# Performance work log

Hardware: AMD Instinct MI355X
Metric: run time of the kernel (lower is better)

## Reference

```python
import jax, jax.numpy as jnp
import numpy as np

N_NODES = 100000
N_EDGES = 1600000
D = 128
N_CLASS = 10
N_LAYERS = 3
BN_EPS = 1e-5


def setup_inputs() -> dict:
    key = jax.random.key(0)
    ks = jax.random.split(key, 12)
    s = 1.0 / np.sqrt(D)
    x = jax.random.normal(ks[0], (N_NODES, D), dtype=jnp.float32)
    edge_index = jax.random.randint(ks[1], (2, N_EDGES), 0, N_NODES, dtype=jnp.int64)
    return {
        "x": x,
        "edge_index": edge_index,
        "W1": jax.random.normal(ks[2], (N_LAYERS, D, D), dtype=jnp.float32) * s,
        "b1": jnp.zeros((N_LAYERS, D), dtype=jnp.float32),
        "gamma": jnp.ones((N_LAYERS, D), dtype=jnp.float32),
        "beta": jnp.zeros((N_LAYERS, D), dtype=jnp.float32),
        "W2": jax.random.normal(ks[3], (N_LAYERS, D, D), dtype=jnp.float32) * s,
        "b2": jnp.zeros((N_LAYERS, D), dtype=jnp.float32),
        "lin1_W": jax.random.normal(ks[4], (D, D), dtype=jnp.float32) * s,
        "lin1_b": jnp.zeros((D,), dtype=jnp.float32),
        "lin2_W": jax.random.normal(ks[5], (N_CLASS, D), dtype=jnp.float32) * s,
        "lin2_b": jnp.zeros((N_CLASS,), dtype=jnp.float32),
    }


def _gin_layer(h, src, dst, W1, b1, g, bt, W2, b2):
    # GINConv with eps=0: mlp((1+eps)*x + sum_{j->i} x_j)
    agg = jax.ops.segment_sum(h[src], dst, num_segments=N_NODES)  # [N, D]
    z = (h + agg) @ W1.T + b1
    # BatchNorm1d (training-mode batch statistics, biased variance)
    mu = jnp.mean(z, axis=0)
    var = jnp.var(z, axis=0)
    z = (z - mu) * jax.lax.rsqrt(var + BN_EPS) * g + bt
    z = jax.nn.relu(z)
    z = jax.nn.relu(z @ W2.T + b2)
    return z


def reference(x, edge_index, W1, b1, gamma, beta, W2, b2, lin1_W, lin1_b, lin2_W, lin2_b):
    src, dst = edge_index[0], edge_index[1]
    h = x.astype(jnp.float32)
    for i in range(N_LAYERS):
        h = _gin_layer(h, src, dst, W1[i], b1[i], gamma[i], beta[i], W2[i], b2[i])
    h = jax.nn.relu(h @ lin1_W.T + lin1_b)
    h = h @ lin2_W.T + lin2_b
    return jax.nn.sigmoid(h)
```

## Files before the change

kernel.cpp:

```cpp
#include <hip/hip_runtime.h>
#include <math.h>

#define N_NODES 100000
#define N_EDGES 1600000
#define D 128
#define NCLASS 10
#define NLAYERS 3
#define BN_EPS 1e-5f

#define LDA 136
#define BUCKET_SH 7
#define NBUK 782
#define NBLK 256
#define CHUNK 6250
#define SCAN_BLKS NBUK

typedef __attribute__((ext_vector_type(8))) short bf16x8;
typedef __attribute__((ext_vector_type(4))) float f32x4;
typedef __attribute__((ext_vector_type(4))) uint u32x4;

__device__ __forceinline__ ushort f2b(float x) {
    uint u = __float_as_uint(x);
    return (ushort)((u + 0x7fffu + ((u >> 16) & 1u)) >> 16);
}
__device__ __forceinline__ float b2f(uint u) {
    return __uint_as_float(u << 16);
}
__device__ __forceinline__ uint pack2(float a, float b) {
    return (uint)f2b(a) | ((uint)f2b(b) << 16);
}

__global__ __launch_bounds__(256) void k_hist(const int* __restrict__ dst,
                                              int* __restrict__ hist) {
    __shared__ int lh[NBUK];
    int t = threadIdx.x, b = blockIdx.x;
    for (int i = t; i < NBUK; i += 256) lh[i] = 0;
    __syncthreads();
    int e0 = b * CHUNK;
    for (int e = e0 + t; e < e0 + CHUNK; e += 256)
        atomicAdd(&lh[dst[e] >> BUCKET_SH], 1);
    __syncthreads();
    for (int i = t; i < NBUK; i += 256) hist[i * NBLK + b] = lh[i];
}

__global__ __launch_bounds__(256) void k_scan1(int* __restrict__ hist, int* __restrict__ psums) {
    __shared__ int sh[256];
    int t = threadIdx.x;
    int i = blockIdx.x * 256 + t;
    int v = hist[i];
    sh[t] = v; __syncthreads();
    for (int off = 1; off < 256; off <<= 1) {
        int a = (t >= off) ? sh[t - off] : 0;
        __syncthreads();
        sh[t] += a;
        __syncthreads();
    }
    hist[i] = sh[t] - v;
    if (t == 255) psums[blockIdx.x] = sh[255];
}

__global__ __launch_bounds__(1024) void k_scan2(int* __restrict__ psums) {
    __shared__ int sh[1024];
    int t = threadIdx.x;
    int v = (t < SCAN_BLKS) ? psums[t] : 0;
    sh[t] = v; __syncthreads();
    for (int off = 1; off < 1024; off <<= 1) {
        int a = (t >= off) ? sh[t - off] : 0;
        __syncthreads();
        sh[t] += a;
        __syncthreads();
    }
    if (t < SCAN_BLKS) psums[t] = sh[t] - v;
}

__global__ __launch_bounds__(256) void k_partition(const int* __restrict__ src,
                                                   const int* __restrict__ dst,
                                                   const int* __restrict__ hist,
                                                   const int* __restrict__ psums,
                                                   uint* __restrict__ tmp) {
    __shared__ int lcur[NBUK];
    int t = threadIdx.x, b = blockIdx.x;
    for (int i = t; i < NBUK; i += 256) lcur[i] = hist[i * NBLK + b] + psums[i];
    __syncthreads();
    int e0 = b * CHUNK;
    for (int e = e0 + t; e < e0 + CHUNK; e += 256) {
        int d = dst[e];
        int bk = d >> BUCKET_SH;
        int pos = atomicAdd(&lcur[bk], 1);
        tmp[pos] = (uint)src[e] | ((uint)(d & ((1 << BUCKET_SH) - 1)) << 17);
    }
}

__global__ __launch_bounds__(256) void k_bucket_fill(const uint* __restrict__ tmp,
                                                     const int* __restrict__ psums,
                                                     int* __restrict__ row_ptr,
                                                     int* __restrict__ csr) {
    __shared__ int hist[128], inc[128], cur[128];
    int b = blockIdx.x, t = threadIdx.x;
    int base = psums[b];
    int end  = (b + 1 < NBUK) ? psums[b + 1] : N_EDGES;
    int nb = end - base;
    int lo = b << BUCKET_SH;
    const uint* bt = tmp + base;

    if (t < 128) hist[t] = 0;
    __syncthreads();
    for (int i = t; i < nb; i += 256)
        atomicAdd(&hist[bt[i] >> 17], 1);
    __syncthreads();
    if (t < 128) inc[t] = hist[t];
    __syncthreads();
    for (int offs = 1; offs < 128; offs <<= 1) {
        int a = (t < 128 && t >= offs) ? inc[t - offs] : 0;
        __syncthreads();
        if (t < 128) inc[t] += a;
        __syncthreads();
    }
    if (t < 128) {
        int node = lo + t;
        if (node < N_NODES) row_ptr[node] = base + inc[t] - hist[t];
        cur[t] = 0;
    }
    if (b == NBUK - 1 && t == 0) row_ptr[N_NODES] = base + nb;
    __syncthreads();
    for (int i = t; i < nb; i += 256) {
        uint u = bt[i];
        int dl = u >> 17;
        int s = (int)(u & 0x1ffffu);
        int p = atomicAdd(&cur[dl], 1);
        csr[base + (inc[dl] - hist[dl]) + p] = s;
    }
}

__global__ void k_conv(const float* __restrict__ x, const float* __restrict__ W1,
                       const float* __restrict__ W2, const float* __restrict__ l1W,
                       ushort* __restrict__ hbf, ushort* __restrict__ wbf) {
    int i = blockIdx.x * 256 + threadIdx.x;
    const int n4x = N_NODES * D / 4;
    if (i < n4x) {
        float4 v = ((const float4*)x)[i];
        uint2 u;
        u.x = pack2(v.x, v.y);
        u.y = pack2(v.z, v.w);
        ((uint2*)hbf)[i] = u;
    } else {
        int k = i - n4x;
        const float* srcp;
        ushort* dstp;
        if (k < 12288)      { srcp = W1 + k * 4;            dstp = wbf + k * 4; }
        else if (k < 24576) { srcp = W2 + (k - 12288) * 4;  dstp = wbf + 49152 + (k - 12288) * 4; }
        else if (k < 28672) { srcp = l1W + (k - 24576) * 4; dstp = wbf + 98304 + (k - 24576) * 4; }
        else return;
        float4 v = *(const float4*)srcp;
        ushort4 u;
        u.x = f2b(v.x); u.y = f2b(v.y); u.z = f2b(v.z); u.w = f2b(v.w);
        *(ushort4*)dstp = u;
    }
}

__global__ __launch_bounds__(256) void k_aggregate(const ushort* __restrict__ hbf,
                                                   const int* __restrict__ row_ptr,
                                                   const int* __restrict__ csr,
                                                   ushort* __restrict__ outbf) {
    int node = blockIdx.x * 4 + (threadIdx.x >> 6);
    int lane = threadIdx.x & 63;
    const uint* hp = (const uint*)hbf;
    uint self = hp[(size_t)node * 64 + lane];
    float ax = b2f(self & 0xffffu), ay = b2f(self >> 16);
    int e0 = row_ptr[node], e1 = row_ptr[node + 1];
    int e = e0;
    for (; e + 7 < e1; e += 8) {
        uint v0 = hp[(size_t)csr[e]     * 64 + lane];
        uint v1 = hp[(size_t)csr[e + 1] * 64 + lane];
        uint v2 = hp[(size_t)csr[e + 2] * 64 + lane];
        uint v3 = hp[(size_t)csr[e + 3] * 64 + lane];
        uint v4 = hp[(size_t)csr[e + 4] * 64 + lane];
        uint v5 = hp[(size_t)csr[e + 5] * 64 + lane];
        uint v6 = hp[(size_t)csr[e + 6] * 64 + lane];
        uint v7 = hp[(size_t)csr[e + 7] * 64 + lane];
        ax += b2f(v0 & 0xffffu); ay += b2f(v0 >> 16);
        ax += b2f(v1 & 0xffffu); ay += b2f(v1 >> 16);
        ax += b2f(v2 & 0xffffu); ay += b2f(v2 >> 16);
        ax += b2f(v3 & 0xffffu); ay += b2f(v3 >> 16);
        ax += b2f(v4 & 0xffffu); ay += b2f(v4 >> 16);
        ax += b2f(v5 & 0xffffu); ay += b2f(v5 >> 16);
        ax += b2f(v6 & 0xffffu); ay += b2f(v6 >> 16);
        ax += b2f(v7 & 0xffffu); ay += b2f(v7 >> 16);
    }
    for (; e < e1; ++e) {
        uint v = hp[(size_t)csr[e] * 64 + lane];
        ax += b2f(v & 0xffffu); ay += b2f(v >> 16);
    }
    __builtin_nontemporal_store(pack2(ax, ay), (uint*)outbf + (size_t)node * 64 + lane);
}

template <int PRE, int POST, int STATS>
__global__ __launch_bounds__(256, 4) void k_gemm(const ushort* __restrict__ inA,
                                                 const ushort* __restrict__ Wbf,
                                                 const float* __restrict__ bias,
                                                 const float* __restrict__ scale,
                                                 const float* __restrict__ shift,
                                                 ushort* __restrict__ outp,
                                                 float* __restrict__ gsum,
                                                 float* __restrict__ gsq,
                                                 int nrows) {
    __shared__ ushort sA[128 * LDA];
    __shared__ float sbias[128];
    __shared__ float lsum[128], lsq[128];

    int t = threadIdx.x;
    int r0 = blockIdx.x * 128;

    if (t < 128) {
        sbias[t] = bias[t];
        lsum[t] = 0.f; lsq[t] = 0.f;
    }

    for (int idx = t; idx < 128 * 16; idx += 256) {
        int r = idx >> 4, c8 = (idx & 15) << 3;
        int rr = r0 + r;
        u32x4 v = (u32x4){0u, 0u, 0u, 0u};
        if (rr < nrows) v = __builtin_nontemporal_load((const u32x4*)(inA + (size_t)rr * 128 + c8));
        if (PRE == 2) {
            float f0 = b2f(v.x & 0xffffu), f1 = b2f(v.x >> 16);
            float f2 = b2f(v.y & 0xffffu), f3 = b2f(v.y >> 16);
            float f4 = b2f(v.z & 0xffffu), f5 = b2f(v.z >> 16);
            float f6 = b2f(v.w & 0xffffu), f7 = b2f(v.w >> 16);
            float4 sc0 = *(const float4*)(scale + c8);
            float4 sc1 = *(const float4*)(scale + c8 + 4);
            float4 sf0 = *(const float4*)(shift + c8);
            float4 sf1 = *(const float4*)(shift + c8 + 4);
            f0 = fmaxf(fmaf(f0, sc0.x, sf0.x), 0.f);
            f1 = fmaxf(fmaf(f1, sc0.y, sf0.y), 0.f);
            f2 = fmaxf(fmaf(f2, sc0.z, sf0.z), 0.f);
            f3 = fmaxf(fmaf(f3, sc0.w, sf0.w), 0.f);
            f4 = fmaxf(fmaf(f4, sc1.x, sf1.x), 0.f);
            f5 = fmaxf(fmaf(f5, sc1.y, sf1.y), 0.f);
            f6 = fmaxf(fmaf(f6, sc1.z, sf1.z), 0.f);
            f7 = fmaxf(fmaf(f7, sc1.w, sf1.w), 0.f);
            v.x = pack2(f0, f1); v.y = pack2(f2, f3);
            v.z = pack2(f4, f5); v.w = pack2(f6, f7);
        }
        *(u32x4*)&sA[r * LDA + c8] = v;
    }
    __syncthreads();

    int lane = t & 63, wid = t >> 6;
    int rl = lane & 15, g = lane >> 4;
    int wr = wid >> 1, wc = wid & 1;

    f32x4 acc[4][4];
#pragma unroll
    for (int i = 0; i < 4; ++i)
#pragma unroll
        for (int j = 0; j < 4; ++j) acc[i][j] = (f32x4){0.f, 0.f, 0.f, 0.f};

#pragma unroll
    for (int ks = 0; ks < 4; ++ks) {
        int koff = ks * 32 + g * 8;
        bf16x8 a[4], b[4];
#pragma unroll
        for (int ni = 0; ni < 4; ++ni)
            b[ni] = *(const bf16x8*)&Wbf[(size_t)(wc * 64 + ni * 16 + rl) * 128 + koff];
#pragma unroll
        for (int mi = 0; mi < 4; ++mi)
            a[mi] = *(const bf16x8*)&sA[(wr * 64 + mi * 16 + rl) * LDA + koff];
#pragma unroll
        for (int mi = 0; mi < 4; ++mi)
#pragma unroll
            for (int ni = 0; ni < 4; ++ni)
                acc[mi][ni] = __builtin_amdgcn_mfma_f32_16x16x32_bf16(a[mi], b[ni], acc[mi][ni], 0, 0, 0);
    }

    float bn[4], ssum[4], ssq[4];
#pragma unroll
    for (int ni = 0; ni < 4; ++ni) {
        bn[ni] = sbias[wc * 64 + ni * 16 + rl];
        ssum[ni] = 0.f; ssq[ni] = 0.f;
    }

#pragma unroll
    for (int mi = 0; mi < 4; ++mi) {
        int orow = r0 + wr * 64 + mi * 16 + g * 4;
#pragma unroll
        for (int j = 0; j < 4; ++j) {
            int row = orow + j;
            if (row < nrows) {
#pragma unroll
                for (int ni = 0; ni < 4; ++ni) {
                    int ocol = wc * 64 + ni * 16 + rl;
                    float o = acc[mi][ni][j] + bn[ni];
                    if (STATS) { ssum[ni] += o; ssq[ni] += o * o; }
                    if (POST) o = fmaxf(o, 0.f);
                    outp[(size_t)row * 128 + ocol] = f2b(o);
                }
            }
        }
    }

    if (STATS) {
#pragma unroll
        for (int ni = 0; ni < 4; ++ni) {
            float s = ssum[ni], q = ssq[ni];
            s += __shfl_xor(s, 16, 64); q += __shfl_xor(q, 16, 64);
            s += __shfl_xor(s, 32, 64); q += __shfl_xor(q, 32, 64);
            if (g == 0) {
                int col = wc * 64 + ni * 16 + rl;
                atomicAdd(&lsum[col], s);
                atomicAdd(&lsq[col], q);
            }
        }
        __syncthreads();
        if (t < 128) {
            atomicAdd(&gsum[t], lsum[t]);
            atomicAdd(&gsq[t], lsq[t]);
        }
    }
}

__global__ void k_bnfin(float* __restrict__ gsum, float* __restrict__ gsq,
                        const float* __restrict__ gamma, const float* __restrict__ beta,
                        float* __restrict__ scale, float* __restrict__ shift) {
    int d = threadIdx.x;
    float s = gsum[d], q = gsq[d];
    float mu = s * (1.f / N_NODES);
    float var = q * (1.f / N_NODES) - mu * mu;
    float rstd = rsqrtf(var + BN_EPS);
    float sc = rstd * gamma[d];
    scale[d] = sc;
    shift[d] = beta[d] - mu * sc;
    gsum[d] = 0.f;
    gsq[d] = 0.f;
}

__global__ __launch_bounds__(256, 3) void k_head(const ushort* __restrict__ hbf,
                                                 const ushort* __restrict__ l1bf,
                                                 const float* __restrict__ b1f,
                                                 const float* __restrict__ W2,
                                                 const float* __restrict__ b2f_,
                                                 float* __restrict__ out) {
    __shared__ ushort sA[128 * LDA];
    __shared__ float sbias[128];
    __shared__ float w2s[NCLASS * 128];
    __shared__ float b2s[NCLASS];

    int t = threadIdx.x;
    int r0 = blockIdx.x * 128;

    if (t < 128) sbias[t] = b1f[t];
    for (int idx = t; idx < (NCLASS * 128) / 4; idx += 256)
        *(float4*)&w2s[idx * 4] = *(const float4*)(W2 + idx * 4);
    if (t < NCLASS) b2s[t] = b2f_[t];

    for (int idx = t; idx < 128 * 16; idx += 256) {
        int r = idx >> 4, c8 = (idx & 15) << 3;
        int rr = r0 + r;
        u32x4 v = (u32x4){0u, 0u, 0u, 0u};
        if (rr < N_NODES) v = __builtin_nontemporal_load((const u32x4*)(hbf + (size_t)rr * 128 + c8));
        *(u32x4*)&sA[r * LDA + c8] = v;
    }
    __syncthreads();

    int lane = t & 63, wid = t >> 6;
    int rl = lane & 15, g = lane >> 4;
    int wr = wid >> 1, wc = wid & 1;

    f32x4 acc[4][4];
#pragma unroll
    for (int i = 0; i < 4; ++i)
#pragma unroll
        for (int j = 0; j < 4; ++j) acc[i][j] = (f32x4){0.f, 0.f, 0.f, 0.f};

#pragma unroll
    for (int ks = 0; ks < 4; ++ks) {
        int koff = ks * 32 + g * 8;
        bf16x8 a[4], b[4];
#pragma unroll
        for (int ni = 0; ni < 4; ++ni)
            b[ni] = *(const bf16x8*)&l1bf[(size_t)(wc * 64 + ni * 16 + rl) * 128 + koff];
#pragma unroll
        for (int mi = 0; mi < 4; ++mi)
            a[mi] = *(const bf16x8*)&sA[(wr * 64 + mi * 16 + rl) * LDA + koff];
#pragma unroll
        for (int mi = 0; mi < 4; ++mi)
#pragma unroll
            for (int ni = 0; ni < 4; ++ni)
                acc[mi][ni] = __builtin_amdgcn_mfma_f32_16x16x32_bf16(a[mi], b[ni], acc[mi][ni], 0, 0, 0);
    }

    __syncthreads();

    float bn[4];
#pragma unroll
    for (int ni = 0; ni < 4; ++ni) bn[ni] = sbias[wc * 64 + ni * 16 + rl];
#pragma unroll
    for (int mi = 0; mi < 4; ++mi) {
        int rowl = wr * 64 + mi * 16 + g * 4;
#pragma unroll
        for (int j = 0; j < 4; ++j) {
#pragma unroll
            for (int ni = 0; ni < 4; ++ni) {
                int ocol = wc * 64 + ni * 16 + rl;
                float o = fmaxf(acc[mi][ni][j] + bn[ni], 0.f);
                sA[ocol * LDA + rowl + j] = f2b(o);
            }
        }
    }
    __syncthreads();

    int row = t & 127, ch = t >> 7;
    float acc2[5] = {0.f, 0.f, 0.f, 0.f, 0.f};
    const float* w2p = &w2s[ch * 5 * 128];
#pragma unroll 4
    for (int k = 0; k < 128; ++k) {
        float v = b2f(sA[k * LDA + row]);
#pragma unroll
        for (int c = 0; c < 5; ++c)
            acc2[c] = fmaf(v, w2p[c * 128 + k], acc2[c]);
    }
    int rr = r0 + row;
    if (rr < N_NODES) {
#pragma unroll
        for (int c = 0; c < 5; ++c) {
            float z = acc2[c] + b2s[ch * 5 + c];
            out[(size_t)rr * NCLASS + ch * 5 + c] = 1.f / (1.f + expf(-z));
        }
    }
}

extern "C" void kernel_launch(void* const* d_in, const int* in_sizes, int n_in,
                              void* d_out, int out_size, void* d_ws, size_t ws_size,
                              hipStream_t stream) {
    const float* x     = (const float*)d_in[0];
    const int*   ei    = (const int*)d_in[1];
    const float* W1    = (const float*)d_in[2];
    const float* b1    = (const float*)d_in[3];
    const float* gamma = (const float*)d_in[4];
    const float* beta  = (const float*)d_in[5];
    const float* W2    = (const float*)d_in[6];
    const float* b2    = (const float*)d_in[7];
    const float* l1W   = (const float*)d_in[8];
    const float* l1b   = (const float*)d_in[9];
    const float* l2W   = (const float*)d_in[10];
    const float* l2b   = (const float*)d_in[11];
    float* out = (float*)d_out;

    char* w = (char*)d_ws;
    ushort* hbf    = (ushort*)(w);
    ushort* zbf    = (ushort*)(w + 25600000);
    ushort* aggout = (ushort*)(w + 51200000);
    int*   row_ptr = (int*)   (w + 76800000);
    int*   csr     = (int*)   (w + 77200640);
    uint*  tmp     = (uint*)  (w + 83600640);
    int*   hist    = (int*)   (w + 90000640);
    int*   psums   = (int*)   (w + 90801920);
    float* gsum    = (float*) (w + 90806016);
    float* gsq     = gsum + 128;
    float* scale   = gsum + 256;
    float* shift   = gsum + 384;
    ushort* wbf    = (ushort*)(w + 90808064);
    ushort* w1bf   = wbf;
    ushort* w2bf   = wbf + 49152;
    ushort* l1bf   = wbf + 98304;

    const int* src = ei;
    const int* dst = ei + N_EDGES;

    const int GEMM_NB = (N_NODES + 127) / 128;

    (void)hipMemsetAsync(gsum, 0, 256 * sizeof(float), stream);

    k_hist<<<NBLK, 256, 0, stream>>>(dst, hist);
    k_scan1<<<SCAN_BLKS, 256, 0, stream>>>(hist, psums);
    k_scan2<<<1, 1024, 0, stream>>>(psums);
    k_partition<<<NBLK, 256, 0, stream>>>(src, dst, hist, psums, tmp);
    k_bucket_fill<<<NBUK, 256, 0, stream>>>(tmp, psums, row_ptr, csr);

    const int CONV_NB = (N_NODES * D / 4 + 28672 + 255) / 256;
    k_conv<<<CONV_NB, 256, 0, stream>>>(x, W1, W2, l1W, hbf, wbf);

    for (int l = 0; l < NLAYERS; ++l) {
        k_aggregate<<<N_NODES / 4, 256, 0, stream>>>(hbf, row_ptr, csr, aggout);
        k_gemm<0, 0, 1><<<GEMM_NB, 256, 0, stream>>>(aggout, w1bf + l * D * D, b1 + l * D,
                                                     nullptr, nullptr, zbf, gsum, gsq, N_NODES);
        k_bnfin<<<1, 128, 0, stream>>>(gsum, gsq, gamma + l * D, beta + l * D, scale, shift);
        k_gemm<2, 1, 0><<<GEMM_NB, 256, 0, stream>>>(zbf, w2bf + l * D * D, b2 + l * D,
                                                     scale, shift, hbf, nullptr, nullptr, N_NODES);
    }

    k_head<<<GEMM_NB, 256, 0, stream>>>(hbf, l1bf, l1b, l2W, l2b, out);
}
```

Measured before the change: 477.3 us.

## Fuse GIN layer GEMMs and BatchNorm via grid-wide barrier in one kernel

Merges the first GEMM with its statistics pass, the BatchNorm finalize, and the second GEMM into a single persistent-style kernel. The z tile stays in registers and LDS while all 782 blocks synchronize through an atomic counter spin barrier, so the bf16 z intermediate is never written to or reread from global memory and two launches per layer go away. This depends on all 782 blocks being co-resident. With __launch_bounds__(256,4) on a 256-CU part that should hold, but a spin barrier without cooperative launch can deadlock if blocks cannot all be scheduled at once.

```diff
diff --git a/kernel.cpp b/kernel.cpp
--- a/kernel.cpp
+++ b/kernel.cpp
@@ -194,25 +194,25 @@
     __builtin_nontemporal_store(pack2(ax, ay), (uint*)outbf + (size_t)node * 64 + lane);
 }
 
-template <int PRE, int POST, int STATS>
-__global__ __launch_bounds__(256, 4) void k_gemm(const ushort* __restrict__ inA,
-                                                 const ushort* __restrict__ Wbf,
-                                                 const float* __restrict__ bias,
-                                                 const float* __restrict__ scale,
-                                                 const float* __restrict__ shift,
-                                                 ushort* __restrict__ outp,
-                                                 float* __restrict__ gsum,
-                                                 float* __restrict__ gsq,
-                                                 int nrows) {
+__global__ __launch_bounds__(256, 4) void k_layer(const ushort* __restrict__ aggin,
+                                                  const ushort* __restrict__ W1bf,
+                                                  const float* __restrict__ b1,
+                                                  const float* __restrict__ gamma,
+                                                  const float* __restrict__ beta,
+                                                  const ushort* __restrict__ W2bf,
+                                                  const float* __restrict__ b2,
+                                                  ushort* __restrict__ hout,
+                                                  float* __restrict__ gsum,
+                                                  float* __restrict__ gsq,
+                                                  int* __restrict__ ctr) {
     __shared__ ushort sA[128 * LDA];
-    __shared__ float sbias[128];
-    __shared__ float lsum[128], lsq[128];
+    __shared__ float sb1[128], sb2[128], lsum[128], lsq[128];
 
     int t = threadIdx.x;
     int r0 = blockIdx.x * 128;
 
     if (t < 128) {
-        sbias[t] = bias[t];
+        sb1[t] = b1[t]; sb2[t] = b2[t];
         lsum[t] = 0.f; lsq[t] = 0.f;
     }
 
@@ -220,27 +220,7 @@
         int r = idx >> 4, c8 = (idx & 15) << 3;
         int rr = r0 + r;
         u32x4 v = (u32x4){0u, 0u, 0u, 0u};
-        if (rr < nrows) v = __builtin_nontemporal_load((const u32x4*)(inA + (size_t)rr * 128 + c8));
-        if (PRE == 2) {
-            float f0 = b2f(v.x & 0xffffu), f1 = b2f(v.x >> 16);
-            float f2 = b2f(v.y & 0xffffu), f3 = b2f(v.y >> 16);
-            float f4 = b2f(v.z & 0xffffu), f5 = b2f(v.z >> 16);
-            float f6 = b2f(v.w & 0xffffu), f7 = b2f(v.w >> 16);
-            float4 sc0 = *(const float4*)(scale + c8);
-            float4 sc1 = *(const float4*)(scale + c8 + 4);
-            float4 sf0 = *(const float4*)(shift + c8);
-            float4 sf1 = *(const float4*)(shift + c8 + 4);
-            f0 = fmaxf(fmaf(f0, sc0.x, sf0.x), 0.f);
-            f1 = fmaxf(fmaf(f1, sc0.y, sf0.y), 0.f);
-            f2 = fmaxf(fmaf(f2, sc0.z, sf0.z), 0.f);
-            f3 = fmaxf(fmaf(f3, sc0.w, sf0.w), 0.f);
-            f4 = fmaxf(fmaf(f4, sc1.x, sf1.x), 0.f);
-            f5 = fmaxf(fmaf(f5, sc1.y, sf1.y), 0.f);
-            f6 = fmaxf(fmaf(f6, sc1.z, sf1.z), 0.f);
-            f7 = fmaxf(fmaf(f7, sc1.w, sf1.w), 0.f);
-            v.x = pack2(f0, f1); v.y = pack2(f2, f3);
-            v.z = pack2(f4, f5); v.w = pack2(f6, f7);
-        }
+        if (rr < N_NODES) v = __builtin_nontemporal_load((const u32x4*)(aggin + (size_t)rr * 128 + c8));
         *(u32x4*)&sA[r * LDA + c8] = v;
     }
     __syncthreads();
@@ -261,7 +241,7 @@
         bf16x8 a[4], b[4];
 #pragma unroll
         for (int ni = 0; ni < 4; ++ni)
-            b[ni] = *(const bf16x8*)&Wbf[(size_t)(wc * 64 + ni * 16 + rl) * 128 + koff];
+            b[ni] = *(const bf16x8*)&W1bf[(size_t)(wc * 64 + ni * 16 + rl) * 128 + koff];
 #pragma unroll
         for (int mi = 0; mi < 4; ++mi)
             a[mi] = *(const bf16x8*)&sA[(wr * 64 + mi * 16 + rl) * LDA + koff];
@@ -272,65 +252,131 @@
                 acc[mi][ni] = __builtin_amdgcn_mfma_f32_16x16x32_bf16(a[mi], b[ni], acc[mi][ni], 0, 0, 0);
     }
 
-    float bn[4], ssum[4], ssq[4];
+    float bn1[4], ssum[4], ssq[4];
 #pragma unroll
     for (int ni = 0; ni < 4; ++ni) {
-        bn[ni] = sbias[wc * 64 + ni * 16 + rl];
+        bn1[ni] = sb1[wc * 64 + ni * 16 + rl];
         ssum[ni] = 0.f; ssq[ni] = 0.f;
     }
-
 #pragma unroll
     for (int mi = 0; mi < 4; ++mi) {
         int orow = r0 + wr * 64 + mi * 16 + g * 4;
 #pragma unroll
         for (int j = 0; j < 4; ++j) {
-            int row = orow + j;
-            if (row < nrows) {
+            if (orow + j < N_NODES) {
 #pragma unroll
                 for (int ni = 0; ni < 4; ++ni) {
-                    int ocol = wc * 64 + ni * 16 + rl;
-                    float o = acc[mi][ni][j] + bn[ni];
-                    if (STATS) { ssum[ni] += o; ssq[ni] += o * o; }
-                    if (POST) o = fmaxf(o, 0.f);
-                    outp[(size_t)row * 128 + ocol] = f2b(o);
+                    float o = acc[mi][ni][j] + bn1[ni];
+                    ssum[ni] += o; ssq[ni] += o * o;
                 }
             }
         }
     }
-
-    if (STATS) {
-#pragma unroll
-        for (int ni = 0; ni < 4; ++ni) {
-            float s = ssum[ni], q = ssq[ni];
-            s += __shfl_xor(s, 16, 64); q += __shfl_xor(q, 16, 64);
-            s += __shfl_xor(s, 32, 64); q += __shfl_xor(q, 32, 64);
-            if (g == 0) {
-                int col = wc * 64 + ni * 16 + rl;
-                atomicAdd(&lsum[col], s);
-                atomicAdd(&lsq[col], q);
+#pragma unroll
+    for (int ni = 0; ni < 4; ++ni) {
+        float s = ssum[ni], q = ssq[ni];
+        s += __shfl_xor(s, 16, 64); q += __shfl_xor(q, 16, 64);
+        s += __shfl_xor(s, 32, 64); q += __shfl_xor(q, 32, 64);
+        if (g == 0) {
+            int col = wc * 64 + ni * 16 + rl;
+            atomicAdd(&lsum[col], s);
+            atomicAdd(&lsq[col], q);
+        }
+    }
+    __syncthreads();
+    if (t < 128) {
+        atomicAdd(&gsum[t], lsum[t]);
+        atomicAdd(&gsq[t], lsq[t]);
+    }
+    __syncthreads();
+
+    if (t == 0) {
+        __hip_atomic_fetch_add(ctr, 1, __ATOMIC_RELEASE, __HIP_MEMORY_SCOPE_AGENT);
+        while (__hip_atomic_load(ctr, __ATOMIC_ACQUIRE, __HIP_MEMORY_SCOPE_AGENT) < NBUK)
+            __builtin_amdgcn_s_sleep(32);
+    }
+    __syncthreads();
+
+    float scl[4], shf[4];
+#pragma unroll
+    for (int ni = 0; ni < 4; ++ni) {
+        int col = wc * 64 + ni * 16 + rl;
+        float s = __hip_atomic_load(&gsum[col], __ATOMIC_RELAXED, __HIP_MEMORY_SCOPE_AGENT);
+        float q = __hip_atomic_load(&gsq[col],  __ATOMIC_RELAXED, __HIP_MEMORY_SCOPE_AGENT);
+        float mu = s * (1.f / N_NODES);
+        float var = q * (1.f / N_NODES) - mu * mu;
+        float rstd = rsqrtf(var + BN_EPS);
+        float sc = rstd * gamma[col];
+        scl[ni] = sc;
+        shf[ni] = beta[col] - mu * sc;
+    }
+
+#pragma unroll
+    for (int mi = 0; mi < 4; ++mi) {
+        int rowl = wr * 64 + mi * 16 + g * 4;
+#pragma unroll
+        for (int j = 0; j < 4; ++j) {
+#pragma unroll
+            for (int ni = 0; ni < 4; ++ni) {
+                int ocol = wc * 64 + ni * 16 + rl;
+                float o = acc[mi][ni][j] + bn1[ni];
+                float v = fmaxf(fmaf(o, scl[ni], shf[ni]), 0.f);
+                sA[(rowl + j) * LDA + ocol] = f2b(v);
             }
         }
-        __syncthreads();
-        if (t < 128) {
-            atomicAdd(&gsum[t], lsum[t]);
-            atomicAdd(&gsq[t], lsq[t]);
-        }
-    }
-}
-
-__global__ void k_bnfin(float* __restrict__ gsum, float* __restrict__ gsq,
-                        const float* __restrict__ gamma, const float* __restrict__ beta,
-                        float* __restrict__ scale, float* __restrict__ shift) {
-    int d = threadIdx.x;
-    float s = gsum[d], q = gsq[d];
-    float mu = s * (1.f / N_NODES);
-    float var = q * (1.f / N_NODES) - mu * mu;
-    float rstd = rsqrtf(var + BN_EPS);
-    float sc = rstd * gamma[d];
-    scale[d] = sc;
-    shift[d] = beta[d] - mu * sc;
-    gsum[d] = 0.f;
-    gsq[d] = 0.f;
+    }
+    __syncthreads();
+
+    f32x4 acc2[4][4];
+#pragma unroll
+    for (int i = 0; i < 4; ++i)
+#pragma unroll
+        for (int j = 0; j < 4; ++j) acc2[i][j] = (f32x4){0.f, 0.f, 0.f, 0.f};
+
+#pragma unroll
+    for (int ks = 0; ks < 4; ++ks) {
+        int koff = ks * 32 + g * 8;
+        bf16x8 a[4], b[4];
+#pragma unroll
+        for (int ni = 0; ni < 4; ++ni)
+            b[ni] = *(const bf16x8*)&W2bf[(size_t)(wc * 64 + ni * 16 + rl) * 128 + koff];
+#pragma unroll
+        for (int mi = 0; mi < 4; ++mi)
+            a[mi] = *(const bf16x8*)&sA[(wr * 64 + mi * 16 + rl) * LDA + koff];
+#pragma unroll
+        for (int mi = 0; mi < 4; ++mi)
+#pragma unroll
+            for (int ni = 0; ni < 4; ++ni)
+                acc2[mi][ni] = __builtin_amdgcn_mfma_f32_16x16x32_bf16(a[mi], b[ni], acc2[mi][ni], 0, 0, 0);
+    }
+    __syncthreads();
+
+    float bn2[4];
+#pragma unroll
+    for (int ni = 0; ni < 4; ++ni) bn2[ni] = sb2[wc * 64 + ni * 16 + rl];
+#pragma unroll
+    for (int mi = 0; mi < 4; ++mi) {
+        int rowl = wr * 64 + mi * 16 + g * 4;
+#pragma unroll
+        for (int j = 0; j < 4; ++j) {
+#pragma unroll
+            for (int ni = 0; ni < 4; ++ni) {
+                int ocol = wc * 64 + ni * 16 + rl;
+                float o = fmaxf(acc2[mi][ni][j] + bn2[ni], 0.f);
+                sA[(rowl + j) * LDA + ocol] = f2b(o);
+            }
+        }
+    }
+    __syncthreads();
+
+    for (int idx = t; idx < 128 * 16; idx += 256) {
+        int r = idx >> 4, c8 = (idx & 15) << 3;
+        int rr = r0 + r;
+        if (rr < N_NODES) {
+            u32x4 v = *(const u32x4*)&sA[r * LDA + c8];
+            __builtin_nontemporal_store(v, (u32x4*)(hout + (size_t)rr * 128 + c8));
+        }
+    }
 }
 
 __global__ __launch_bounds__(256, 3) void k_head(const ushort* __restrict__ hbf,
@@ -447,18 +493,15 @@
 
     char* w = (char*)d_ws;
     ushort* hbf    = (ushort*)(w);
-    ushort* zbf    = (ushort*)(w + 25600000);
-    ushort* aggout = (ushort*)(w + 51200000);
-    int*   row_ptr = (int*)   (w + 76800000);
-    int*   csr     = (int*)   (w + 77200640);
-    uint*  tmp     = (uint*)  (w + 83600640);
-    int*   hist    = (int*)   (w + 90000640);
-    int*   psums   = (int*)   (w + 90801920);
-    float* gsum    = (float*) (w + 90806016);
-    float* gsq     = gsum + 128;
-    float* scale   = gsum + 256;
-    float* shift   = gsum + 384;
-    ushort* wbf    = (ushort*)(w + 90808064);
+    ushort* aggout = (ushort*)(w + 25600000);
+    int*   row_ptr = (int*)   (w + 51200000);
+    int*   csr     = (int*)   (w + 51600640);
+    uint*  tmp     = (uint*)  (w + 58000640);
+    int*   hist    = (int*)   (w + 64400640);
+    int*   psums   = (int*)   (w + 65201920);
+    float* gstats  = (float*) (w + 65206016);
+    int*   ctrs    = (int*)   (w + 65209088);
+    ushort* wbf    = (ushort*)(w + 65209472);
     ushort* w1bf   = wbf;
     ushort* w2bf   = wbf + 49152;
     ushort* l1bf   = wbf + 98304;
@@ -466,9 +509,7 @@
     const int* src = ei;
     const int* dst = ei + N_EDGES;
 
-    const int GEMM_NB = (N_NODES + 127) / 128;
-
-    (void)hipMemsetAsync(gsum, 0, 256 * sizeof(float), stream);
+    (void)hipMemsetAsync(gstats, 0, 3072 + 64, stream);
 
     k_hist<<<NBLK, 256, 0, stream>>>(dst, hist);
     k_scan1<<<SCAN_BLKS, 256, 0, stream>>>(hist, psums);
@@ -481,12 +522,12 @@
 
     for (int l = 0; l < NLAYERS; ++l) {
         k_aggregate<<<N_NODES / 4, 256, 0, stream>>>(hbf, row_ptr, csr, aggout);
-        k_gemm<0, 0, 1><<<GEMM_NB, 256, 0, stream>>>(aggout, w1bf + l * D * D, b1 + l * D,
-                                                     nullptr, nullptr, zbf, gsum, gsq, N_NODES);
-        k_bnfin<<<1, 128, 0, stream>>>(gsum, gsq, gamma + l * D, beta + l * D, scale, shift);
-        k_gemm<2, 1, 0><<<GEMM_NB, 256, 0, stream>>>(zbf, w2bf + l * D * D, b2 + l * D,
-                                                     scale, shift, hbf, nullptr, nullptr, N_NODES);
-    }
-
-    k_head<<<GEMM_NB, 256, 0, stream>>>(hbf, l1bf, l1b, l2W, l2b, out);
-}
+        k_layer<<<NBUK, 256, 0, stream>>>(aggout, w1bf + l * D * D, b1 + l * D,
+                                          gamma + l * D, beta + l * D,
+                                          w2bf + l * D * D, b2 + l * D,
+                                          hbf, gstats + l * 256, gstats + l * 256 + 128,
+                                          ctrs + l);
+    }
+
+    k_head<<<NBUK, 256, 0, stream>>>(hbf, l1bf, l1b, l2W, l2b, out);
+}
```

New measurement: 585.1 us. +22.6%, slower.

## Fold BN finalize into second GEMM and stage GEMM output through LDS

Applied to the files above, without the earlier changes.

Drops the separate single-block BN finalize kernel. Each block of the second GEMM now recomputes scale and shift from the global sums into shared memory, and each layer gets its own stats buffer, all zeroed once at the start. The GEMM epilogue now writes bf16 results into shared memory and then stores whole rows with coalesced 16-byte nontemporal stores, replacing scattered 2-byte global stores. The cost is extra __syncthreads and redundant per-block BN arithmetic.

```diff
diff --git a/kernel.cpp b/kernel.cpp
--- a/kernel.cpp
+++ b/kernel.cpp
@@ -198,8 +198,8 @@
 __global__ __launch_bounds__(256, 4) void k_gemm(const ushort* __restrict__ inA,
                                                  const ushort* __restrict__ Wbf,
                                                  const float* __restrict__ bias,
-                                                 const float* __restrict__ scale,
-                                                 const float* __restrict__ shift,
+                                                 const float* __restrict__ gamma,
+                                                 const float* __restrict__ beta,
                                                  ushort* __restrict__ outp,
                                                  float* __restrict__ gsum,
                                                  float* __restrict__ gsq,
@@ -207,14 +207,25 @@
     __shared__ ushort sA[128 * LDA];
     __shared__ float sbias[128];
     __shared__ float lsum[128], lsq[128];
+    __shared__ float sscale[128], sshift[128];
 
     int t = threadIdx.x;
     int r0 = blockIdx.x * 128;
 
     if (t < 128) {
         sbias[t] = bias[t];
-        lsum[t] = 0.f; lsq[t] = 0.f;
-    }
+        if (STATS) { lsum[t] = 0.f; lsq[t] = 0.f; }
+        if (PRE == 2) {
+            float s = gsum[t], q = gsq[t];
+            float mu = s * (1.f / N_NODES);
+            float var = q * (1.f / N_NODES) - mu * mu;
+            float rstd = rsqrtf(var + BN_EPS);
+            float sc = rstd * gamma[t];
+            sscale[t] = sc;
+            sshift[t] = beta[t] - mu * sc;
+        }
+    }
+    if (PRE == 2) __syncthreads();
 
     for (int idx = t; idx < 128 * 16; idx += 256) {
         int r = idx >> 4, c8 = (idx & 15) << 3;
@@ -226,10 +237,10 @@
             float f2 = b2f(v.y & 0xffffu), f3 = b2f(v.y >> 16);
             float f4 = b2f(v.z & 0xffffu), f5 = b2f(v.z >> 16);
             float f6 = b2f(v.w & 0xffffu), f7 = b2f(v.w >> 16);
-            float4 sc0 = *(const float4*)(scale + c8);
-            float4 sc1 = *(const float4*)(scale + c8 + 4);
-            float4 sf0 = *(const float4*)(shift + c8);
-            float4 sf1 = *(const float4*)(shift + c8 + 4);
+            float4 sc0 = *(const float4*)&sscale[c8];
+            float4 sc1 = *(const float4*)&sscale[c8 + 4];
+            float4 sf0 = *(const float4*)&sshift[c8];
+            float4 sf1 = *(const float4*)&sshift[c8 + 4];
             f0 = fmaxf(fmaf(f0, sc0.x, sf0.x), 0.f);
             f1 = fmaxf(fmaf(f1, sc0.y, sf0.y), 0.f);
             f2 = fmaxf(fmaf(f2, sc0.z, sf0.z), 0.f);
@@ -271,6 +282,7 @@
             for (int ni = 0; ni < 4; ++ni)
                 acc[mi][ni] = __builtin_amdgcn_mfma_f32_16x16x32_bf16(a[mi], b[ni], acc[mi][ni], 0, 0, 0);
     }
+    __syncthreads();
 
     float bn[4], ssum[4], ssq[4];
 #pragma unroll
@@ -281,19 +293,17 @@
 
 #pragma unroll
     for (int mi = 0; mi < 4; ++mi) {
-        int orow = r0 + wr * 64 + mi * 16 + g * 4;
+        int rowl = wr * 64 + mi * 16 + g * 4;
 #pragma unroll
         for (int j = 0; j < 4; ++j) {
-            int row = orow + j;
-            if (row < nrows) {
-#pragma unroll
-                for (int ni = 0; ni < 4; ++ni) {
-                    int ocol = wc * 64 + ni * 16 + rl;
-                    float o = acc[mi][ni][j] + bn[ni];
-                    if (STATS) { ssum[ni] += o; ssq[ni] += o * o; }
-                    if (POST) o = fmaxf(o, 0.f);
-                    outp[(size_t)row * 128 + ocol] = f2b(o);
-                }
+            bool inb = (r0 + rowl + j) < nrows;
+#pragma unroll
+            for (int ni = 0; ni < 4; ++ni) {
+                int ocol = wc * 64 + ni * 16 + rl;
+                float o = acc[mi][ni][j] + bn[ni];
+                if (STATS && inb) { ssum[ni] += o; ssq[ni] += o * o; }
+                if (POST) o = fmaxf(o, 0.f);
+                sA[(rowl + j) * LDA + ocol] = f2b(o);
             }
         }
     }
@@ -310,27 +320,21 @@
                 atomicAdd(&lsq[col], q);
             }
         }
-        __syncthreads();
-        if (t < 128) {
-            atomicAdd(&gsum[t], lsum[t]);
-            atomicAdd(&gsq[t], lsq[t]);
-        }
-    }
-}
-
-__global__ void k_bnfin(float* __restrict__ gsum, float* __restrict__ gsq,
-                        const float* __restrict__ gamma, const float* __restrict__ beta,
-                        float* __restrict__ scale, float* __restrict__ shift) {
-    int d = threadIdx.x;
-    float s = gsum[d], q = gsq[d];
-    float mu = s * (1.f / N_NODES);
-    float var = q * (1.f / N_NODES) - mu * mu;
-    float rstd = rsqrtf(var + BN_EPS);
-    float sc = rstd * gamma[d];
-    scale[d] = sc;
-    shift[d] = beta[d] - mu * sc;
-    gsum[d] = 0.f;
-    gsq[d] = 0.f;
+    }
+    __syncthreads();
+
+    for (int idx = t; idx < 128 * 16; idx += 256) {
+        int r = idx >> 4, c8 = (idx & 15) << 3;
+        int rr = r0 + r;
+        if (rr < nrows) {
+            u32x4 v = *(const u32x4*)&sA[r * LDA + c8];
+            __builtin_nontemporal_store(v, (u32x4*)(outp + (size_t)rr * 128 + c8));
+        }
+    }
+    if (STATS && t < 128) {
+        atomicAdd(&gsum[t], lsum[t]);
+        atomicAdd(&gsq[t], lsq[t]);
+    }
 }
 
 __global__ __launch_bounds__(256, 3) void k_head(const ushort* __restrict__ hbf,
@@ -454,11 +458,8 @@
     uint*  tmp     = (uint*)  (w + 83600640);
     int*   hist    = (int*)   (w + 90000640);
     int*   psums   = (int*)   (w + 90801920);
-    float* gsum    = (float*) (w + 90806016);
-    float* gsq     = gsum + 128;
-    float* scale   = gsum + 256;
-    float* shift   = gsum + 384;
-    ushort* wbf    = (ushort*)(w + 90808064);
+    float* gstats  = (float*) (w + 90806016);
+    ushort* wbf    = (ushort*)(w + 90809344);
     ushort* w1bf   = wbf;
     ushort* w2bf   = wbf + 49152;
     ushort* l1bf   = wbf + 98304;
@@ -466,9 +467,7 @@
     const int* src = ei;
     const int* dst = ei + N_EDGES;
 
-    const int GEMM_NB = (N_NODES + 127) / 128;
-
-    (void)hipMemsetAsync(gsum, 0, 256 * sizeof(float), stream);
+    (void)hipMemsetAsync(gstats, 0, 3072, stream);
 
     k_hist<<<NBLK, 256, 0, stream>>>(dst, hist);
     k_scan1<<<SCAN_BLKS, 256, 0, stream>>>(hist, psums);
@@ -480,13 +479,15 @@
     k_conv<<<CONV_NB, 256, 0, stream>>>(x, W1, W2, l1W, hbf, wbf);
 
     for (int l = 0; l < NLAYERS; ++l) {
+        float* gsum = gstats + l * 256;
+        float* gsq  = gsum + 128;
         k_aggregate<<<N_NODES / 4, 256, 0, stream>>>(hbf, row_ptr, csr, aggout);
-        k_gemm<0, 0, 1><<<GEMM_NB, 256, 0, stream>>>(aggout, w1bf + l * D * D, b1 + l * D,
-                                                     nullptr, nullptr, zbf, gsum, gsq, N_NODES);
-        k_bnfin<<<1, 128, 0, stream>>>(gsum, gsq, gamma + l * D, beta + l * D, scale, shift);
-        k_gemm<2, 1, 0><<<GEMM_NB, 256, 0, stream>>>(zbf, w2bf + l * D * D, b2 + l * D,
-                                                     scale, shift, hbf, nullptr, nullptr, N_NODES);
-    }
-
-    k_head<<<GEMM_NB, 256, 0, stream>>>(hbf, l1bf, l1b, l2W, l2b, out);
-}
+        k_gemm<0, 0, 1><<<NBUK, 256, 0, stream>>>(aggout, w1bf + l * D * D, b1 + l * D,
+                                                  nullptr, nullptr, zbf, gsum, gsq, N_NODES);
+        k_gemm<2, 1, 0><<<NBUK, 256, 0, stream>>>(zbf, w2bf + l * D * D, b2 + l * D,
+                                                  gamma + l * D, beta + l * D, hbf,
+                                                  gsum, gsq, N_NODES);
+    }
+
+    k_head<<<NBUK, 256, 0, stream>>>(hbf, l1bf, l1b, l2W, l2b, out);
+}
```

Result: no change. 476.9 us (-0.1%).
